# Kernel optimization log

Hardware: AMD Instinct MI355X
Metric: run time of the kernel (lower is better)

The kernel has to match this reference:

```python
import jax, jax.numpy as jnp
import numpy as np

B, S, H, D, E = 4, 2048, 16, 64, 1024
BASE_SCALE = 0.03125  # config.base_scale = 1/sqrt(n_embed)
SQK_INIT_VAL = 1.0


def setup_inputs() -> dict:
    key = jax.random.key(0)
    ks = jax.random.split(key, 5)
    x = jax.random.normal(ks[0], (B, S, E), dtype=jnp.float32)
    Wq = jax.random.normal(ks[1], (E, E), dtype=jnp.float32) * 0.02
    Wk = jax.random.normal(ks[2], (E, E), dtype=jnp.float32) * 0.02
    Wv = jax.random.normal(ks[3], (E, E), dtype=jnp.float32) * 0.02
    sqk = BASE_SCALE * jnp.ones((E,), dtype=jnp.float32)
    # RoPE frequencies: theta = 10000^(-2i/D), angles[s, i] = s * theta_i
    theta = 1.0 / (10000.0 ** (np.arange(0, D, 2, dtype=np.float32) / D))  # [D/2]
    angles = np.arange(S, dtype=np.float32)[:, None] * theta[None, :]       # [S, D/2]
    freqs_cos = jnp.asarray(np.cos(angles), dtype=jnp.float32)
    freqs_sin = jnp.asarray(np.sin(angles), dtype=jnp.float32)
    return {"x": x, "Wq": Wq, "Wk": Wk, "Wv": Wv, "sqk": sqk,
            "freqs_cos": freqs_cos, "freqs_sin": freqs_sin}


def _rope(t, cos, sin):
    # t: [B, S, H, D]; cos/sin: [S, D/2] broadcast as [1, S, 1, D/2]
    tr = t.reshape(*t.shape[:-1], D // 2, 2)
    a, b = tr[..., 0], tr[..., 1]
    c = cos[None, :, None, :]
    s = sin[None, :, None, :]
    out = jnp.stack([a * c - b * s, a * s + b * c], axis=-1)
    return out.reshape(t.shape)


def _l2norm(t):
    return t / jnp.linalg.norm(t, axis=-1, keepdims=True)


def reference(x, Wq, Wk, Wv, sqk, freqs_cos, freqs_sin):
    # Linear (torch: x @ W.T), no bias
    q = jnp.einsum('bse,oe->bso', x, Wq).reshape(B, S, H, D)
    k = jnp.einsum('bse,oe->bso', x, Wk).reshape(B, S, H, D)
    v = jnp.einsum('bse,oe->bso', x, Wv).reshape(B, S, H, D)
    q = _rope(q, freqs_cos, freqs_sin)
    k = _rope(k, freqs_cos, freqs_sin)
    # -> [B, H, S, D]
    q = q.transpose(0, 2, 1, 3)
    k = k.transpose(0, 2, 1, 3)
    v = v.transpose(0, 2, 1, 3)
    scale = (sqk * (SQK_INIT_VAL / BASE_SCALE)).reshape(1, H, 1, D)
    q = scale * _l2norm(q)
    k = scale * _l2norm(k)
    scores = jnp.einsum('bhqd,bhkd->bhqk', q, k) * (D ** -0.5)
    attn = jax.nn.softmax(scores, axis=-1)
    out = jnp.einsum('bhqk,bhkd->bhqd', attn, v)  # [B, H, S, D]
    return out.transpose(0, 2, 1, 3).reshape(B, S, E)
```

## Files before the change

### kernel.cpp

```cpp
#include <hip/hip_runtime.h>
#include <stdint.h>

#define B_ 4
#define S_ 2048
#define H_ 16
#define D_ 64
#define E_ 1024

typedef __bf16 bf16x8 __attribute__((ext_vector_type(8)));
typedef float f32x4 __attribute__((ext_vector_type(4)));
typedef unsigned short u16x4 __attribute__((ext_vector_type(4)));

static __device__ __forceinline__ unsigned short f2bf(float f) {
    unsigned u = __builtin_bit_cast(unsigned, f);
    u += 0x7fffu + ((u >> 16) & 1u);
    return (unsigned short)(u >> 16);
}

static __device__ __forceinline__ float fexp2(float x) {
    float r;
    asm("v_exp_f32 %0, %1" : "=v"(r) : "v"(x));
    return r;
}

static __device__ __forceinline__ unsigned cvtpk_bf16(float lo, float hi) {
    unsigned r;
    asm("v_cvt_pk_bf16_f32 %0, %1, %2" : "=v"(r) : "v"(lo), "v"(hi));
    return r;
}

static __device__ __forceinline__ f32x4 mfma16(bf16x8 a, bf16x8 b, f32x4 c) {
    return __builtin_amdgcn_mfma_f32_16x16x32_bf16(a, b, c, 0, 0, 0);
}

static __device__ __forceinline__ void gload_lds16(const void* g, void* l) {
    __builtin_amdgcn_global_load_lds(
        (__attribute__((address_space(1))) void*)g,
        (__attribute__((address_space(3))) void*)l, 16, 0, 0);
}

__global__ void cvt_f32_bf16_k(const float* __restrict__ src,
                               unsigned short* __restrict__ dst, int n4) {
    int stride = gridDim.x * blockDim.x;
    for (int i = blockIdx.x * blockDim.x + threadIdx.x; i < n4; i += stride) {
        float4 v = reinterpret_cast<const float4*>(src)[i];
        u16x4 o;
        o[0] = f2bf(v.x); o[1] = f2bf(v.y); o[2] = f2bf(v.z); o[3] = f2bf(v.w);
        reinterpret_cast<u16x4*>(dst)[i] = o;
    }
}

__global__ __launch_bounds__(256) void qkv_gemm_k(
    const unsigned short* __restrict__ xbf,
    const unsigned short* __restrict__ wbf,
    const float* __restrict__ sqk,
    const float* __restrict__ fcos,
    const float* __restrict__ fsin,
    unsigned short* __restrict__ qws,
    unsigned short* __restrict__ kws,
    unsigned short* __restrict__ vtws)
{
    __shared__ unsigned short As[128 * 32];
    __shared__ unsigned short Bs[128 * 32];
    const int tid = threadIdx.x;
    const int w = tid >> 6, lane = tid & 63;
    const int wr = w >> 1, wc = w & 1;
    const int mbase = blockIdx.y * 128;
    const int nbase = blockIdx.x * 128;
    const int c15 = lane & 15;
    const int g4 = lane >> 4;
    const int kb8 = g4 * 8;

    const f32x4 zero4 = {0.f, 0.f, 0.f, 0.f};
    f32x4 acc[4][4];
#pragma unroll
    for (int m = 0; m < 4; m++)
#pragma unroll
        for (int n = 0; n < 4; n++) acc[m][n] = zero4;

    for (int kt = 0; kt < 32; ++kt) {
        const int k0 = kt * 32;
#pragma unroll
        for (int i = 0; i < 2; i++) {
            int g = (i * 4 + w) * 64 + lane;
            int row = g >> 2, slot = g & 3;
            gload_lds16(xbf + (size_t)(mbase + row) * E_ + k0 + slot * 8,
                        As + (i * 4 + w) * 512);
            gload_lds16(wbf + (size_t)(nbase + row) * E_ + k0 + slot * 8,
                        Bs + (i * 4 + w) * 512);
        }
        asm volatile("s_waitcnt vmcnt(0)" ::: "memory");
        __syncthreads();
        bf16x8 af[4], bfr[4];
#pragma unroll
        for (int m = 0; m < 4; m++)
            af[m] = *(const bf16x8*)(As + (wr * 64 + m * 16 + c15) * 32 + kb8);
#pragma unroll
        for (int n = 0; n < 4; n++)
            bfr[n] = *(const bf16x8*)(Bs + (wc * 64 + n * 16 + c15) * 32 + kb8);
#pragma unroll
        for (int m = 0; m < 4; m++)
#pragma unroll
            for (int n = 0; n < 4; n++)
                acc[m][n] = mfma16(af[m], bfr[n], acc[m][n]);
        __syncthreads();
    }

    const int gcb = nbase + wc * 64;
    const int qkv = gcb >> 10;
    const int oo = gcb & 1023;
    const int h = oo >> 6;

    if (qkv < 2) {
        unsigned short* dst = (qkv == 0) ? qws : kws;
        const float qs = (qkv == 0) ? (0.125f * 1.44269504f) : 1.0f;
        float cs4[4];
#pragma unroll
        for (int n = 0; n < 4; n++)
            cs4[n] = sqk[oo + n * 16 + c15] * 32.0f * qs;
#pragma unroll
        for (int m = 0; m < 4; m++) {
#pragma unroll
            for (int r = 0; r < 4; r++) {
                const int grow = mbase + wr * 64 + m * 16 + g4 * 4 + r;
                const int bb = grow >> 11;
                const int srow = grow & 2047;
                float nv[4], ss = 0.f;
#pragma unroll
                for (int n = 0; n < 4; n++) {
                    const int d = n * 16 + c15;
                    const float a = acc[m][n][r];
                    const float other = __shfl_xor(a, 1);
                    const float cc = fcos[srow * 32 + (d >> 1)];
                    const float sn = fsin[srow * 32 + (d >> 1)];
                    const float rv = (d & 1) ? (other * sn + a * cc) : (a * cc - other * sn);
                    nv[n] = rv;
                    ss += rv * rv;
                }
#pragma unroll
                for (int mask = 1; mask < 16; mask <<= 1)
                    ss += __shfl_xor(ss, mask);
                const float rn = rsqrtf(ss);
                unsigned short* rp = dst + ((size_t)(bb * H_ + h) * S_ + srow) * D_;
#pragma unroll
                for (int n = 0; n < 4; n++)
                    rp[n * 16 + c15] = f2bf(nv[n] * rn * cs4[n]);
            }
        }
    } else {
#pragma unroll
        for (int m = 0; m < 4; m++) {
            const int grow0 = mbase + wr * 64 + m * 16 + g4 * 4;
            const int bb = grow0 >> 11;
            const int srow0 = grow0 & 2047;
#pragma unroll
            for (int n = 0; n < 4; n++) {
                const int d = n * 16 + c15;
                u16x4 pk;
#pragma unroll
                for (int r = 0; r < 4; r++) pk[r] = f2bf(acc[m][n][r]);
                *reinterpret_cast<u16x4*>(vtws + ((size_t)(bb * H_ + h) * D_ + d) * S_ + srow0) = pk;
            }
        }
    }
}

__global__ __launch_bounds__(512) void attn_fwd_k(
    const unsigned short* __restrict__ qws,
    const unsigned short* __restrict__ kws,
    const unsigned short* __restrict__ vtws,
    float* __restrict__ out)
{
    __shared__ unsigned short Klds[2 * 64 * 64];
    __shared__ unsigned short Vlds[2 * 64 * 64];
    __shared__ unsigned short Plds[128 * 68];
    const int tid = threadIdx.x;
    const int w = tid >> 6, lane = tid & 63;
    const int c15 = lane & 15;
    const int g4 = lane >> 4;
    const int kb8 = g4 * 8;

    const int id = blockIdx.x;
    const int xcd = id & 7, c = id >> 3;
    const int bh = xcd * 8 + (c >> 4);
    const int q0 = (c & 15) * 128;
    const int b = bh >> 4, h = bh & 15;

    bf16x8 qf[2];
    {
        const unsigned short* qp =
            qws + ((size_t)bh * S_ + (q0 + w * 16 + c15)) * D_ + kb8;
        qf[0] = *(const bf16x8*)qp;
        qf[1] = *(const bf16x8*)(qp + 32);
    }

    const f32x4 zero4 = {0.f, 0.f, 0.f, 0.f};
    float mrow[4], lrow[4];
    f32x4 o[4];
#pragma unroll
    for (int n = 0; n < 4; n++) o[n] = zero4;
#pragma unroll
    for (int r = 0; r < 4; r++) { mrow[r] = -3.0e38f; lrow[r] = 0.f; }

    const char* kbase_g = (const char*)(kws + (size_t)bh * S_ * D_);
    const unsigned short* vbase_g = vtws + (size_t)bh * D_ * S_;

    auto STAGE = [&](int t, int bsel) {
        {
            int loff = (w * 64 + lane) * 16;
            int soff = loff ^ (((loff >> 7) & 7) << 4);
            gload_lds16(kbase_g + (size_t)t * 8192 + soff,
                        (char*)Klds + bsel * 8192 + w * 1024);
        }
        {
            int g = w * 64 + lane;
            int row = g >> 3, slot = g & 7;
            int soff = (slot * 16) ^ ((row & 7) << 4);
            gload_lds16((const char*)(vbase_g + (size_t)row * S_ + t * 64) + soff,
                        (char*)Vlds + bsel * 8192 + w * 1024);
        }
    };

    STAGE(0, 0);
    asm volatile("s_waitcnt vmcnt(0)" ::: "memory");
    __syncthreads();

    int cur = 0;
    for (int kt = 0; kt < 32; ++kt) {
        if (kt + 1 < 32) STAGE(kt + 1, cur ^ 1);

        const char* kb_l = (const char*)Klds + cur * 8192;
        const char* vb_l = (const char*)Vlds + cur * 8192;

        f32x4 sf[4];
        bf16x8 kf[4][2];
#pragma unroll
        for (int n = 0; n < 4; n++) {
            const int kvc = n * 16 + c15;
            const char* kro = kb_l + kvc * 128;
            const int sw = (kvc & 7) << 4;
            kf[n][0] = *(const bf16x8*)(kro + ((kb8 * 2) ^ sw));
            kf[n][1] = *(const bf16x8*)(kro + ((kb8 * 2 + 64) ^ sw));
        }
        __builtin_amdgcn_s_setprio(1);
#pragma unroll
        for (int n = 0; n < 4; n++) {
            sf[n] = zero4;
            sf[n] = mfma16(qf[0], kf[n][0], sf[n]);
            sf[n] = mfma16(qf[1], kf[n][1], sf[n]);
        }
        __builtin_amdgcn_s_setprio(0);

        float pmax[4];
#pragma unroll
        for (int r = 0; r < 4; r++)
            pmax[r] = fmaxf(fmaxf(sf[0][r], sf[1][r]), fmaxf(sf[2][r], sf[3][r]));
        int ok = (pmax[0] <= mrow[0] + 8.0f) & (pmax[1] <= mrow[1] + 8.0f) &
                 (pmax[2] <= mrow[2] + 8.0f) & (pmax[3] <= mrow[3] + 8.0f);
        if (!__all(ok)) {
#pragma unroll
            for (int r = 0; r < 4; r++) {
                float mn = pmax[r];
#pragma unroll
                for (int mask = 1; mask < 16; mask <<= 1)
                    mn = fmaxf(mn, __shfl_xor(mn, mask));
                float mt = fmaxf(mrow[r], mn);
                float al = fexp2(mrow[r] - mt);
                mrow[r] = mt;
                lrow[r] *= al;
#pragma unroll
                for (int n = 0; n < 4; n++) o[n][r] *= al;
            }
        }
#pragma unroll
        for (int n = 0; n < 4; n++)
#pragma unroll
            for (int r = 0; r < 4; r++)
                sf[n][r] = fexp2(sf[n][r] - mrow[r]);
#pragma unroll
        for (int r = 0; r < 4; r++)
            lrow[r] += (sf[0][r] + sf[1][r]) + (sf[2][r] + sf[3][r]);

        {
            const int pr0 = w * 16 + g4 * 4;
#pragma unroll
            for (int r = 0; r < 4; r++) {
                unsigned w01 = cvtpk_bf16(sf[0][r], sf[1][r]);
                unsigned w23 = cvtpk_bf16(sf[2][r], sf[3][r]);
                unsigned short* row = Plds + (pr0 + r) * 68;
                row[c15] = (unsigned short)w01;
                row[16 + c15] = (unsigned short)(w01 >> 16);
                row[32 + c15] = (unsigned short)w23;
                row[48 + c15] = (unsigned short)(w23 >> 16);
            }
        }
        asm volatile("s_waitcnt lgkmcnt(0)" ::: "memory");

        bf16x8 pf[2];
        {
            const unsigned short* pp = Plds + (w * 16 + c15) * 68 + kb8;
            pf[0] = *(const bf16x8*)pp;
            pf[1] = *(const bf16x8*)(pp + 32);
        }
        bf16x8 vf[4][2];
#pragma unroll
        for (int n = 0; n < 4; n++) {
            const int dc = n * 16 + c15;
            const char* vro = vb_l + dc * 128;
            const int sw = (dc & 7) << 4;
            vf[n][0] = *(const bf16x8*)(vro + ((kb8 * 2) ^ sw));
            vf[n][1] = *(const bf16x8*)(vro + ((kb8 * 2 + 64) ^ sw));
        }
        __builtin_amdgcn_s_setprio(1);
#pragma unroll
        for (int n = 0; n < 4; n++) {
            o[n] = mfma16(pf[0], vf[n][0], o[n]);
            o[n] = mfma16(pf[1], vf[n][1], o[n]);
        }
        __builtin_amdgcn_s_setprio(0);

        if (kt + 1 < 32) {
            asm volatile("s_waitcnt vmcnt(0)" ::: "memory");
            __syncthreads();
            cur ^= 1;
        }
    }

#pragma unroll
    for (int mask = 1; mask < 16; mask <<= 1)
#pragma unroll
        for (int r = 0; r < 4; r++)
            lrow[r] += __shfl_xor(lrow[r], mask);

    const int so0 = q0 + w * 16 + g4 * 4;
#pragma unroll
    for (int r = 0; r < 4; r++) {
        const float inv = 1.0f / lrow[r];
        float* op = out + ((size_t)b * S_ + so0 + r) * E_ + h * D_;
#pragma unroll
        for (int n = 0; n < 4; n++)
            op[n * 16 + c15] = o[n][r] * inv;
    }
}

extern "C" void kernel_launch(void* const* d_in, const int* in_sizes, int n_in,
                              void* d_out, int out_size, void* d_ws, size_t ws_size,
                              hipStream_t stream) {
    (void)in_sizes; (void)n_in; (void)out_size; (void)ws_size;
    const float* x = (const float*)d_in[0];
    const float* Wq = (const float*)d_in[1];
    const float* Wk = (const float*)d_in[2];
    const float* Wv = (const float*)d_in[3];
    const float* sqk = (const float*)d_in[4];
    const float* fcos = (const float*)d_in[5];
    const float* fsin = (const float*)d_in[6];

    char* ws = (char*)d_ws;
    size_t off = 0;
    unsigned short* xbf = (unsigned short*)(ws + off); off += (size_t)B_ * S_ * E_ * 2;
    unsigned short* wbf = (unsigned short*)(ws + off); off += (size_t)3 * E_ * E_ * 2;
    unsigned short* qws = (unsigned short*)(ws + off); off += (size_t)B_ * H_ * S_ * D_ * 2;
    unsigned short* kws = (unsigned short*)(ws + off); off += (size_t)B_ * H_ * S_ * D_ * 2;
    unsigned short* vtws = (unsigned short*)(ws + off); off += (size_t)B_ * H_ * S_ * D_ * 2;

    cvt_f32_bf16_k<<<dim3(2048), dim3(256), 0, stream>>>(x, xbf, (B_ * S_ * E_) / 4);
    cvt_f32_bf16_k<<<dim3(512), dim3(256), 0, stream>>>(Wq, wbf, (E_ * E_) / 4);
    cvt_f32_bf16_k<<<dim3(512), dim3(256), 0, stream>>>(Wk, wbf + E_ * E_, (E_ * E_) / 4);
    cvt_f32_bf16_k<<<dim3(512), dim3(256), 0, stream>>>(Wv, wbf + 2 * E_ * E_, (E_ * E_) / 4);

    qkv_gemm_k<<<dim3(24, 64), dim3(256), 0, stream>>>(xbf, wbf, sqk, fcos, fsin,
                                                       qws, kws, vtws);
    attn_fwd_k<<<dim3(1024), dim3(512), 0, stream>>>(qws, kws, vtws, (float*)d_out);
}
```

Before: 334.1 us.

## Load K/V fragments directly from global memory instead of LDS staging

Removes the double-buffered LDS staging of K and V tiles and the per-iteration barrier, so each wave loads its MFMA operand fragments straight from global memory. The goal is to eliminate block-wide synchronisation and LDS traffic. In exchange, every wave redundantly fetches the same K/V tiles through the cache hierarchy. Global load latency is also no longer prefetched one tile ahead.

```diff
diff --git a/kernel.cpp b/kernel.cpp
--- a/kernel.cpp
+++ b/kernel.cpp
@@ -171,8 +171,6 @@
     const unsigned short* __restrict__ vtws,
     float* __restrict__ out)
 {
-    __shared__ unsigned short Klds[2 * 64 * 64];
-    __shared__ unsigned short Vlds[2 * 64 * 64];
     __shared__ unsigned short Plds[128 * 68];
     const int tid = threadIdx.x;
     const int w = tid >> 6, lane = tid & 63;
@@ -202,52 +200,25 @@
 #pragma unroll
     for (int r = 0; r < 4; r++) { mrow[r] = -3.0e38f; lrow[r] = 0.f; }
 
-    const char* kbase_g = (const char*)(kws + (size_t)bh * S_ * D_);
-    const unsigned short* vbase_g = vtws + (size_t)bh * D_ * S_;
-
-    auto STAGE = [&](int t, int bsel) {
-        {
-            int loff = (w * 64 + lane) * 16;
-            int soff = loff ^ (((loff >> 7) & 7) << 4);
-            gload_lds16(kbase_g + (size_t)t * 8192 + soff,
-                        (char*)Klds + bsel * 8192 + w * 1024);
-        }
-        {
-            int g = w * 64 + lane;
-            int row = g >> 3, slot = g & 7;
-            int soff = (slot * 16) ^ ((row & 7) << 4);
-            gload_lds16((const char*)(vbase_g + (size_t)row * S_ + t * 64) + soff,
-                        (char*)Vlds + bsel * 8192 + w * 1024);
-        }
-    };
-
-    STAGE(0, 0);
-    asm volatile("s_waitcnt vmcnt(0)" ::: "memory");
-    __syncthreads();
-
-    int cur = 0;
+    const unsigned short* kbase = kws + (size_t)bh * S_ * D_;
+    const unsigned short* vbase = vtws + (size_t)bh * D_ * S_;
+
     for (int kt = 0; kt < 32; ++kt) {
-        if (kt + 1 < 32) STAGE(kt + 1, cur ^ 1);
-
-        const char* kb_l = (const char*)Klds + cur * 8192;
-        const char* vb_l = (const char*)Vlds + cur * 8192;
+        const unsigned short* kp = kbase + ((size_t)(kt * 64 + c15)) * D_ + kb8;
+        bf16x8 kf0[4], kf1[4];
+#pragma unroll
+        for (int n = 0; n < 4; n++) {
+            kf0[n] = *(const bf16x8*)(kp + n * 16 * D_);
+            kf1[n] = *(const bf16x8*)(kp + n * 16 * D_ + 32);
+        }
 
         f32x4 sf[4];
-        bf16x8 kf[4][2];
-#pragma unroll
-        for (int n = 0; n < 4; n++) {
-            const int kvc = n * 16 + c15;
-            const char* kro = kb_l + kvc * 128;
-            const int sw = (kvc & 7) << 4;
-            kf[n][0] = *(const bf16x8*)(kro + ((kb8 * 2) ^ sw));
-            kf[n][1] = *(const bf16x8*)(kro + ((kb8 * 2 + 64) ^ sw));
-        }
         __builtin_amdgcn_s_setprio(1);
 #pragma unroll
         for (int n = 0; n < 4; n++) {
             sf[n] = zero4;
-            sf[n] = mfma16(qf[0], kf[n][0], sf[n]);
-            sf[n] = mfma16(qf[1], kf[n][1], sf[n]);
+            sf[n] = mfma16(qf[0], kf0[n], sf[n]);
+            sf[n] = mfma16(qf[1], kf1[n], sf[n]);
         }
         __builtin_amdgcn_s_setprio(0);
 
@@ -280,6 +251,14 @@
 #pragma unroll
         for (int r = 0; r < 4; r++)
             lrow[r] += (sf[0][r] + sf[1][r]) + (sf[2][r] + sf[3][r]);
+
+        const unsigned short* vp = vbase + (size_t)c15 * S_ + kt * 64 + kb8;
+        bf16x8 vf0[4], vf1[4];
+#pragma unroll
+        for (int n = 0; n < 4; n++) {
+            vf0[n] = *(const bf16x8*)(vp + (size_t)n * 16 * S_);
+            vf1[n] = *(const bf16x8*)(vp + (size_t)n * 16 * S_ + 32);
+        }
 
         {
             const int pr0 = w * 16 + g4 * 4;
@@ -302,28 +281,13 @@
             pf[0] = *(const bf16x8*)pp;
             pf[1] = *(const bf16x8*)(pp + 32);
         }
-        bf16x8 vf[4][2];
+        __builtin_amdgcn_s_setprio(1);
 #pragma unroll
         for (int n = 0; n < 4; n++) {
-            const int dc = n * 16 + c15;
-            const char* vro = vb_l + dc * 128;
-            const int sw = (dc & 7) << 4;
-            vf[n][0] = *(const bf16x8*)(vro + ((kb8 * 2) ^ sw));
-            vf[n][1] = *(const bf16x8*)(vro + ((kb8 * 2 + 64) ^ sw));
-        }
-        __builtin_amdgcn_s_setprio(1);
-#pragma unroll
-        for (int n = 0; n < 4; n++) {
-            o[n] = mfma16(pf[0], vf[n][0], o[n]);
-            o[n] = mfma16(pf[1], vf[n][1], o[n]);
+            o[n] = mfma16(pf[0], vf0[n], o[n]);
+            o[n] = mfma16(pf[1], vf1[n], o[n]);
         }
         __builtin_amdgcn_s_setprio(0);
-
-        if (kt + 1 < 32) {
-            asm volatile("s_waitcnt vmcnt(0)" ::: "memory");
-            __syncthreads();
-            cur ^= 1;
-        }
     }
 
 #pragma unroll
```

New measurement: 635.0 us. 90.1% more time.
